# Kernel tuning notes

Hardware: AMD Instinct MI355X
Metric: run time of the kernel (lower is better)

The kernel has to match this reference:

```python
import jax, jax.numpy as jnp
import numpy as np

B, NX, NY = 16, 1024, 1024


def _grad(f, axis):
    # torch.gradient(f, dim=axis, edge_order=2), unit spacing
    fm = jnp.moveaxis(f, axis, -1)
    g = (jnp.roll(fm, -1, -1) - jnp.roll(fm, 1, -1)) * 0.5
    g0 = (-3.0 * fm[..., 0] + 4.0 * fm[..., 1] - fm[..., 2]) * 0.5
    gN = (3.0 * fm[..., -1] - 4.0 * fm[..., -2] + fm[..., -3]) * 0.5
    g = g.at[..., 0].set(g0).at[..., -1].set(gN)
    return jnp.moveaxis(g, -1, axis)


def _grad2(f, axis):
    # roll-based second derivative with one-sided 2nd-order boundary stencils
    fm = jnp.moveaxis(f, axis, -1)
    g = jnp.roll(fm, -1, -1) - 2.0 * fm + jnp.roll(fm, 1, -1)
    g0 = 2.0 * fm[..., 0] - 5.0 * fm[..., 1] + 4.0 * fm[..., 2] - fm[..., 3]
    gN = 2.0 * fm[..., -1] - 5.0 * fm[..., -2] + 4.0 * fm[..., -3] - fm[..., -4]
    g = g.at[..., 0].set(g0).at[..., -1].set(gN)
    return jnp.moveaxis(g, -1, axis)


def setup_inputs() -> dict:
    key = jax.random.key(0)
    k1, k2, k3, k4 = jax.random.split(key, 4)
    f = jax.random.uniform(k1, (B, NX, NY), dtype=jnp.float32)
    A_grid = jax.random.normal(k2, (2, NX, NY), dtype=jnp.float32)
    B_grid = jax.random.uniform(k3, (3, NX, NY), dtype=jnp.float32)
    dt = jax.random.uniform(k4, (B,), dtype=jnp.float32)
    return {"f": f, "A_grid": A_grid, "B_grid": B_grid, "dt": dt}


def reference(f, A_grid, B_grid, dt):
    # Af: [B,2,NX,NY], Bf: [B,3,NX,NY]
    Af = A_grid[None] * f[:, None]
    Bf = B_grid[None] * f[:, None]
    gradv_Af = _grad(Af[:, 0], 1) + _grad(Af[:, 1], 2)
    gradvv_Bf = (
        _grad2(Bf[:, 0], 1)
        + _grad2(Bf[:, 1], 2)
        + _grad(_grad(Bf[:, 2], 2), 1)
        + _grad(_grad(Bf[:, 2], 1), 2)
    )
    df = -gradv_Af + gradvv_Bf * 0.5
    f_new = f + df * dt[:, None, None]
    # ensure_non_negative_f=True
    return jnp.maximum(f_new, 0.0)
```

## Files before the change

### kernel.cpp

```cpp
#include <hip/hip_runtime.h>

#define BATCH 16
#define NX 1024
#define NY 1024
#define CHUNK 8
#define NB 2
#define PLANE (NX * NY)

typedef float v4f __attribute__((ext_vector_type(4)));

struct RawS { v4f a0, a1, b0, b1, b2; float a1l, b1l, b2l, a1r, b1r, b2r; };
struct RawF { v4f f; float fl, fr; };
struct Halo { float a1m, b1m, b2m, a1p, b1p, b2p; };
struct Row  { float pa[4], rr[4], tt[4], fc[4], yc[4]; };

__device__ __forceinline__ RawS load_rawS(int xx, int y0, int tid,
    const float* __restrict__ A0, const float* __restrict__ A1,
    const float* __restrict__ B0, const float* __restrict__ B1,
    const float* __restrict__ B2)
{
    const int base = xx * NY + y0;
    RawS r;
    r.a0 = *(const v4f*)(A0 + base);
    r.a1 = *(const v4f*)(A1 + base);
    r.b0 = *(const v4f*)(B0 + base);
    r.b1 = *(const v4f*)(B1 + base);
    r.b2 = *(const v4f*)(B2 + base);
    const int lane = tid & 63;
    const bool nl = (lane == 0)  && (tid > 0);
    const bool nr = (lane == 63) && (tid < 255);
    r.a1l = nl ? A1[base - 1] : 0.0f;
    r.b1l = nl ? B1[base - 1] : 0.0f;
    r.b2l = nl ? B2[base - 1] : 0.0f;
    r.a1r = nr ? A1[base + 4] : 0.0f;
    r.b1r = nr ? B1[base + 4] : 0.0f;
    r.b2r = nr ? B2[base + 4] : 0.0f;
    return r;
}

__device__ __forceinline__ RawF load_rawF(int xx, int y0, int tid,
    const float* __restrict__ fb)
{
    const int base = xx * NY + y0;
    RawF r;
    r.f = *(const v4f*)(fb + base);
    const int lane = tid & 63;
    const bool nl = (lane == 0)  && (tid > 0);
    const bool nr = (lane == 63) && (tid < 255);
    r.fl = nl ? fb[base - 1] : 0.0f;
    r.fr = nr ? fb[base + 4] : 0.0f;
    return r;
}

__device__ __forceinline__ Halo make_halo(const RawS& rs, int tid)
{
    const int lane = tid & 63;
    Halo h;
    h.a1m = __shfl_up(rs.a1.w, 1);   h.b1m = __shfl_up(rs.b1.w, 1);
    h.b2m = __shfl_up(rs.b2.w, 1);
    h.a1p = __shfl_down(rs.a1.x, 1); h.b1p = __shfl_down(rs.b1.x, 1);
    h.b2p = __shfl_down(rs.b2.x, 1);
    if (lane == 0)  { h.a1m = rs.a1l; h.b1m = rs.b1l; h.b2m = rs.b2l; }
    if (lane == 63) { h.a1p = rs.a1r; h.b1p = rs.b1r; h.b2p = rs.b2r; }
    return h;
}

__device__ __forceinline__ Row convert(const RawS& rs, const Halo& h,
                                       const RawF& rf, int tid)
{
    const int lane = tid & 63;
    float fm = __shfl_up(rf.f.w, 1);
    float fp = __shfl_down(rf.f.x, 1);
    if (lane == 0)  fm = rf.fl;
    if (lane == 63) fp = rf.fr;

    const float qe[6] = { h.a1m * fm, rs.a1.x * rf.f.x, rs.a1.y * rf.f.y,
                          rs.a1.z * rf.f.z, rs.a1.w * rf.f.w, h.a1p * fp };
    const float se[6] = { h.b1m * fm, rs.b1.x * rf.f.x, rs.b1.y * rf.f.y,
                          rs.b1.z * rf.f.z, rs.b1.w * rf.f.w, h.b1p * fp };
    const float te[6] = { h.b2m * fm, rs.b2.x * rf.f.x, rs.b2.y * rf.f.y,
                          rs.b2.z * rf.f.z, rs.b2.w * rf.f.w, h.b2p * fp };

    Row o;
    o.fc[0] = rf.f.x; o.fc[1] = rf.f.y; o.fc[2] = rf.f.z; o.fc[3] = rf.f.w;
    o.pa[0] = rs.a0.x * rf.f.x; o.pa[1] = rs.a0.y * rf.f.y;
    o.pa[2] = rs.a0.z * rf.f.z; o.pa[3] = rs.a0.w * rf.f.w;
    o.rr[0] = rs.b0.x * rf.f.x; o.rr[1] = rs.b0.y * rf.f.y;
    o.rr[2] = rs.b0.z * rf.f.z; o.rr[3] = rs.b0.w * rf.f.w;

    #pragma unroll
    for (int i = 0; i < 4; ++i) {
        const float dq  = 0.5f * (qe[i + 2] - qe[i]);
        const float d2s = se[i + 2] - 2.0f * se[i + 1] + se[i];
        o.tt[i] = 0.5f * (te[i + 2] - te[i]);
        o.yc[i] = -dq + 0.5f * d2s;
    }
    if (tid == 0) {
        const float dq  = 0.5f * (-3.0f * qe[1] + 4.0f * qe[2] - qe[3]);
        const float d2s = 2.0f * se[1] - 5.0f * se[2] + 4.0f * se[3] - se[4];
        o.tt[0] = 0.5f * (-3.0f * te[1] + 4.0f * te[2] - te[3]);
        o.yc[0] = -dq + 0.5f * d2s;
    }
    if (tid == 255) {
        const float dq  = 0.5f * (3.0f * qe[4] - 4.0f * qe[3] + qe[2]);
        const float d2s = 2.0f * se[4] - 5.0f * se[3] + 4.0f * se[2] - se[1];
        o.tt[3] = 0.5f * (3.0f * te[4] - 4.0f * te[3] + te[2]);
        o.yc[3] = -dq + 0.5f * d2s;
    }
    return o;
}

__global__ __launch_bounds__(256) void fp2d_kernel(
    const float* __restrict__ f,
    const float* __restrict__ Ag,
    const float* __restrict__ Bg,
    const float* __restrict__ dt,
    float* __restrict__ out)
{
    const int tid = threadIdx.x;
    const int y0  = tid * 4;
    const int x0  = blockIdx.x * CHUNK;
    const int bb  = blockIdx.y * NB;

    const float* __restrict__ A0 = Ag;
    const float* __restrict__ A1 = Ag + PLANE;
    const float* __restrict__ B0 = Bg;
    const float* __restrict__ B1 = Bg + PLANE;
    const float* __restrict__ B2 = Bg + 2 * PLANE;

    const float* fb[NB];
    float* ob[NB];
    float dtb[NB];
    #pragma unroll
    for (int j = 0; j < NB; ++j) {
        fb[j]  = f   + (size_t)(bb + j) * PLANE;
        ob[j]  = out + (size_t)(bb + j) * PLANE;
        dtb[j] = dt[bb + j];
    }

    const int cs = (x0 == 0) ? 1 : x0;
    const int ce = (x0 + CHUNK == NX) ? NX - 2 : x0 + CHUNK - 1;

    {
    }
    RawS sM = load_rawS(cs - 1, y0, tid, A0, A1, B0, B1, B2);
    RawS sC = load_rawS(cs,     y0, tid, A0, A1, B0, B1, B2);
    RawS sP = load_rawS(cs + 1, y0, tid, A0, A1, B0, B1, B2);
    RawF fM[NB], fC[NB], fP[NB];
    #pragma unroll
    for (int j = 0; j < NB; ++j) {
        fM[j] = load_rawF(cs - 1, y0, tid, fb[j]);
        fC[j] = load_rawF(cs,     y0, tid, fb[j]);
        fP[j] = load_rawF(cs + 1, y0, tid, fb[j]);
    }
    Halo hM = make_halo(sM, tid);
    Halo hC = make_halo(sC, tid);
    Row m[NB], c[NB];
    #pragma unroll
    for (int j = 0; j < NB; ++j) {
        m[j] = convert(sM, hM, fM[j], tid);
        c[j] = convert(sC, hC, fC[j], tid);
    }

    for (int x = cs; x <= ce; ++x) {
        const int xn = (x + 2 < NX) ? x + 2 : NX - 1;
        RawS sN = load_rawS(xn, y0, tid, A0, A1, B0, B1, B2);
        RawF fN[NB];
        #pragma unroll
        for (int j = 0; j < NB; ++j) fN[j] = load_rawF(xn, y0, tid, fb[j]);

        Halo hP = make_halo(sP, tid);
        #pragma unroll
        for (int j = 0; j < NB; ++j) {
            Row p = convert(sP, hP, fP[j], tid);
            v4f o;
            #pragma unroll
            for (int i = 0; i < 4; ++i) {
                const float dxP   = 0.5f * (p.pa[i] - m[j].pa[i]);
                const float dxxR  = p.rr[i] - 2.0f * c[j].rr[i] + m[j].rr[i];
                const float dxdyT = 0.5f * (p.tt[i] - m[j].tt[i]);
                const float df = -dxP + c[j].yc[i] + 0.5f * dxxR + dxdyT;
                o[i] = fmaxf(c[j].fc[i] + df * dtb[j], 0.0f);
            }
            __builtin_nontemporal_store(o, (v4f*)(ob[j] + x * NY + y0));
            m[j] = c[j]; c[j] = p;
        }
        sP = sN;
        #pragma unroll
        for (int j = 0; j < NB; ++j) fP[j] = fN[j];
    }

    if (x0 == 0) {
        RawS s0 = load_rawS(0, y0, tid, A0, A1, B0, B1, B2);
        RawS s1 = load_rawS(1, y0, tid, A0, A1, B0, B1, B2);
        RawS s2 = load_rawS(2, y0, tid, A0, A1, B0, B1, B2);
        RawS s3 = load_rawS(3, y0, tid, A0, A1, B0, B1, B2);
        Halo h0 = make_halo(s0, tid), h1 = make_halo(s1, tid);
        Halo h2 = make_halo(s2, tid), h3 = make_halo(s3, tid);
        #pragma unroll
        for (int j = 0; j < NB; ++j) {
            Row r0 = convert(s0, h0, load_rawF(0, y0, tid, fb[j]), tid);
            Row r1 = convert(s1, h1, load_rawF(1, y0, tid, fb[j]), tid);
            Row r2 = convert(s2, h2, load_rawF(2, y0, tid, fb[j]), tid);
            Row r3 = convert(s3, h3, load_rawF(3, y0, tid, fb[j]), tid);
            v4f o;
            #pragma unroll
            for (int i = 0; i < 4; ++i) {
                const float dxP   = 0.5f * (-3.0f * r0.pa[i] + 4.0f * r1.pa[i] - r2.pa[i]);
                const float dxxR  = 2.0f * r0.rr[i] - 5.0f * r1.rr[i] + 4.0f * r2.rr[i] - r3.rr[i];
                const float dxdyT = 0.5f * (-3.0f * r0.tt[i] + 4.0f * r1.tt[i] - r2.tt[i]);
                const float df = -dxP + r0.yc[i] + 0.5f * dxxR + dxdyT;
                o[i] = fmaxf(r0.fc[i] + df * dtb[j], 0.0f);
            }
            __builtin_nontemporal_store(o, (v4f*)(ob[j] + y0));
        }
    }

    if (x0 + CHUNK == NX) {
        RawS s0 = load_rawS(NX - 1, y0, tid, A0, A1, B0, B1, B2);
        RawS s1 = load_rawS(NX - 2, y0, tid, A0, A1, B0, B1, B2);
        RawS s2 = load_rawS(NX - 3, y0, tid, A0, A1, B0, B1, B2);
        RawS s3 = load_rawS(NX - 4, y0, tid, A0, A1, B0, B1, B2);
        Halo h0 = make_halo(s0, tid), h1 = make_halo(s1, tid);
        Halo h2 = make_halo(s2, tid), h3 = make_halo(s3, tid);
        #pragma unroll
        for (int j = 0; j < NB; ++j) {
            Row r0 = convert(s0, h0, load_rawF(NX - 1, y0, tid, fb[j]), tid);
            Row r1 = convert(s1, h1, load_rawF(NX - 2, y0, tid, fb[j]), tid);
            Row r2 = convert(s2, h2, load_rawF(NX - 3, y0, tid, fb[j]), tid);
            Row r3 = convert(s3, h3, load_rawF(NX - 4, y0, tid, fb[j]), tid);
            v4f o;
            #pragma unroll
            for (int i = 0; i < 4; ++i) {
                const float dxP   = 0.5f * (3.0f * r0.pa[i] - 4.0f * r1.pa[i] + r2.pa[i]);
                const float dxxR  = 2.0f * r0.rr[i] - 5.0f * r1.rr[i] + 4.0f * r2.rr[i] - r3.rr[i];
                const float dxdyT = 0.5f * (3.0f * r0.tt[i] - 4.0f * r1.tt[i] + r2.tt[i]);
                const float df = -dxP + r0.yc[i] + 0.5f * dxxR + dxdyT;
                o[i] = fmaxf(r0.fc[i] + df * dtb[j], 0.0f);
            }
            __builtin_nontemporal_store(o, (v4f*)(ob[j] + (NX - 1) * NY + y0));
        }
    }
}

extern "C" void kernel_launch(void* const* d_in, const int* in_sizes, int n_in,
                              void* d_out, int out_size, void* d_ws, size_t ws_size,
                              hipStream_t stream) {
    const float* f  = (const float*)d_in[0];
    const float* Ag = (const float*)d_in[1];
    const float* Bg = (const float*)d_in[2];
    const float* dt = (const float*)d_in[3];
    float* out = (float*)d_out;

    dim3 block(256, 1, 1);
    dim3 grid(NX / CHUNK, BATCH / NB, 1);
    fp2d_kernel<<<grid, block, 0, stream>>>(f, Ag, Bg, dt, out);
}
```

Baseline: 147.5 us.

## Refactor stencil into per-row coefficient form with direct halo loads

Recasts the interior stencil algebraically: per grid row it precomputes combined coefficients from A/B once, shared across the batch, then produces three partial contributions per f row (ep, es, en) that are summed across x with a single fma. This cuts the per-element multiplies and the carried state. Halo values are now loaded directly from memory with clamped indices instead of using wave shuffles plus lane-edge fallback loads, and f is read with nontemporal loads. The risks are more scalar global loads per row, extra coefficient registers, and slightly different floating-point rounding from the reassociated sums.

New measurement: 169.6 us. 15.0% more time.

```diff
diff --git a/kernel.cpp b/kernel.cpp
--- a/kernel.cpp
+++ b/kernel.cpp
@@ -9,85 +9,117 @@
 
 typedef float v4f __attribute__((ext_vector_type(4)));
 
-struct RawS { v4f a0, a1, b0, b1, b2; float a1l, b1l, b2l, a1r, b1r, b2r; };
-struct RawF { v4f f; float fl, fr; };
-struct Halo { float a1m, b1m, b2m, a1p, b1p, b2p; };
-struct Row  { float pa[4], rr[4], tt[4], fc[4], yc[4]; };
-
-__device__ __forceinline__ RawS load_rawS(int xx, int y0, int tid,
+struct RawG { v4f a0, a1, b0, b1, b2; float a1m, a1p, b1m, b1p, b2m, b2p; };
+struct RawFv { v4f f; float fm, fp; };
+struct Coef { float cp[4], cm[4], c0x[4], xp[4], xm[4], b2w[6], K[4], T[3]; };
+struct RowI { float ep[4], es[4], en[4], fc[4]; };
+struct RowB { float pa[4], rr[4], tt[4], yc[4], fc[4]; };
+
+__device__ __forceinline__ RawG load_rawG(int xx, int y0, int ymo, int ypo,
     const float* __restrict__ A0, const float* __restrict__ A1,
     const float* __restrict__ B0, const float* __restrict__ B1,
     const float* __restrict__ B2)
 {
-    const int base = xx * NY + y0;
-    RawS r;
-    r.a0 = *(const v4f*)(A0 + base);
-    r.a1 = *(const v4f*)(A1 + base);
-    r.b0 = *(const v4f*)(B0 + base);
-    r.b1 = *(const v4f*)(B1 + base);
-    r.b2 = *(const v4f*)(B2 + base);
-    const int lane = tid & 63;
-    const bool nl = (lane == 0)  && (tid > 0);
-    const bool nr = (lane == 63) && (tid < 255);
-    r.a1l = nl ? A1[base - 1] : 0.0f;
-    r.b1l = nl ? B1[base - 1] : 0.0f;
-    r.b2l = nl ? B2[base - 1] : 0.0f;
-    r.a1r = nr ? A1[base + 4] : 0.0f;
-    r.b1r = nr ? B1[base + 4] : 0.0f;
-    r.b2r = nr ? B2[base + 4] : 0.0f;
+    const int b = xx * NY;
+    RawG r;
+    r.a0 = *(const v4f*)(A0 + b + y0);
+    r.a1 = *(const v4f*)(A1 + b + y0);
+    r.b0 = *(const v4f*)(B0 + b + y0);
+    r.b1 = *(const v4f*)(B1 + b + y0);
+    r.b2 = *(const v4f*)(B2 + b + y0);
+    r.a1m = A1[b + ymo]; r.b1m = B1[b + ymo]; r.b2m = B2[b + ymo];
+    r.a1p = A1[b + ypo]; r.b1p = B1[b + ypo]; r.b2p = B2[b + ypo];
     return r;
 }
 
-__device__ __forceinline__ RawF load_rawF(int xx, int y0, int tid,
-    const float* __restrict__ fb)
-{
-    const int base = xx * NY + y0;
-    RawF r;
-    r.f = *(const v4f*)(fb + base);
-    const int lane = tid & 63;
-    const bool nl = (lane == 0)  && (tid > 0);
-    const bool nr = (lane == 63) && (tid < 255);
-    r.fl = nl ? fb[base - 1] : 0.0f;
-    r.fr = nr ? fb[base + 4] : 0.0f;
+__device__ __forceinline__ RawFv load_f(int xx, int y0, int ymo, int ypo,
+                                        const float* __restrict__ fb)
+{
+    const int b = xx * NY;
+    RawFv r;
+    r.f  = __builtin_nontemporal_load((const v4f*)(fb + b + y0));
+    r.fm = __builtin_nontemporal_load(fb + b + ymo);
+    r.fp = __builtin_nontemporal_load(fb + b + ypo);
     return r;
 }
 
-__device__ __forceinline__ Halo make_halo(const RawS& rs, int tid)
-{
-    const int lane = tid & 63;
-    Halo h;
-    h.a1m = __shfl_up(rs.a1.w, 1);   h.b1m = __shfl_up(rs.b1.w, 1);
-    h.b2m = __shfl_up(rs.b2.w, 1);
-    h.a1p = __shfl_down(rs.a1.x, 1); h.b1p = __shfl_down(rs.b1.x, 1);
-    h.b2p = __shfl_down(rs.b2.x, 1);
-    if (lane == 0)  { h.a1m = rs.a1l; h.b1m = rs.b1l; h.b2m = rs.b2l; }
-    if (lane == 63) { h.a1p = rs.a1r; h.b1p = rs.b1r; h.b2p = rs.b2r; }
-    return h;
-}
-
-__device__ __forceinline__ Row convert(const RawS& rs, const Halo& h,
-                                       const RawF& rf, int tid)
-{
-    const int lane = tid & 63;
-    float fm = __shfl_up(rf.f.w, 1);
-    float fp = __shfl_down(rf.f.x, 1);
-    if (lane == 0)  fm = rf.fl;
-    if (lane == 63) fp = rf.fr;
-
-    const float qe[6] = { h.a1m * fm, rs.a1.x * rf.f.x, rs.a1.y * rf.f.y,
-                          rs.a1.z * rf.f.z, rs.a1.w * rf.f.w, h.a1p * fp };
-    const float se[6] = { h.b1m * fm, rs.b1.x * rf.f.x, rs.b1.y * rf.f.y,
-                          rs.b1.z * rf.f.z, rs.b1.w * rf.f.w, h.b1p * fp };
-    const float te[6] = { h.b2m * fm, rs.b2.x * rf.f.x, rs.b2.y * rf.f.y,
-                          rs.b2.z * rf.f.z, rs.b2.w * rf.f.w, h.b2p * fp };
-
-    Row o;
-    o.fc[0] = rf.f.x; o.fc[1] = rf.f.y; o.fc[2] = rf.f.z; o.fc[3] = rf.f.w;
-    o.pa[0] = rs.a0.x * rf.f.x; o.pa[1] = rs.a0.y * rf.f.y;
-    o.pa[2] = rs.a0.z * rf.f.z; o.pa[3] = rs.a0.w * rf.f.w;
-    o.rr[0] = rs.b0.x * rf.f.x; o.rr[1] = rs.b0.y * rf.f.y;
-    o.rr[2] = rs.b0.z * rf.f.z; o.rr[3] = rs.b0.w * rf.f.w;
-
+__device__ __forceinline__ Coef make_coef(const RawG& g, int tid)
+{
+    Coef c;
+    const float a1w[6] = { g.a1m, g.a1.x, g.a1.y, g.a1.z, g.a1.w, g.a1p };
+    const float b1w[6] = { g.b1m, g.b1.x, g.b1.y, g.b1.z, g.b1.w, g.b1p };
+    c.b2w[0] = g.b2m; c.b2w[1] = g.b2.x; c.b2w[2] = g.b2.y;
+    c.b2w[3] = g.b2.z; c.b2w[4] = g.b2.w; c.b2w[5] = g.b2p;
+    #pragma unroll
+    for (int e = 0; e < 4; ++e) {
+        c.xp[e]  = 0.5f * (g.b0[e] - g.a0[e]);
+        c.xm[e]  = 0.5f * (g.b0[e] + g.a0[e]);
+        c.c0x[e] = -(g.b0[e] + b1w[e + 1]);
+        c.cp[e]  = 0.5f * (b1w[e + 2] - a1w[e + 2]);
+        c.cm[e]  = 0.5f * (a1w[e]     + b1w[e]);
+    }
+    if (tid == 0) {
+        c.K[0] = -g.b0.x + 1.5f * g.a1.x + g.b1.x;
+        c.K[1] = -2.0f * g.a1.y - 2.5f * g.b1.y;
+        c.K[2] =  0.5f * g.a1.z + 2.0f * g.b1.z;
+        c.K[3] = -0.5f * g.b1.w;
+        c.T[0] = -0.75f * g.b2.x; c.T[1] = g.b2.y; c.T[2] = -0.25f * g.b2.z;
+    }
+    if (tid == 255) {
+        c.K[0] = -g.b0.w - 1.5f * g.a1.w + g.b1.w;
+        c.K[1] =  2.0f * g.a1.z - 2.5f * g.b1.z;
+        c.K[2] = -0.5f * g.a1.y + 2.0f * g.b1.y;
+        c.K[3] = -0.5f * g.b1.x;
+        c.T[0] = 0.75f * g.b2.w; c.T[1] = -g.b2.z; c.T[2] = 0.25f * g.b2.y;
+    }
+    return c;
+}
+
+__device__ __forceinline__ RowI convertI(const Coef& cf, const RawFv& rf, int tid)
+{
+    const float fw[6] = { rf.fm, rf.f.x, rf.f.y, rf.f.z, rf.f.w, rf.fp };
+    float te[6];
+    #pragma unroll
+    for (int w = 0; w < 6; ++w) te[w] = cf.b2w[w] * fw[w];
+    RowI o;
+    #pragma unroll
+    for (int e = 0; e < 4; ++e) {
+        const float d = 0.25f * (te[e + 2] - te[e]);
+        o.fc[e] = fw[e + 1];
+        o.ep[e] = fw[e + 1] * cf.xp[e]  + d;
+        o.en[e] = fw[e + 1] * cf.xm[e]  - d;
+        o.es[e] = fw[e + 1] * cf.c0x[e] + cf.cp[e] * fw[e + 2] + cf.cm[e] * fw[e];
+    }
+    if (tid == 0) {
+        o.es[0] = cf.K[0] * fw[1] + cf.K[1] * fw[2] + cf.K[2] * fw[3] + cf.K[3] * fw[4];
+        const float h = cf.T[0] * fw[1] + cf.T[1] * fw[2] + cf.T[2] * fw[3];
+        o.ep[0] = fw[1] * cf.xp[0] + h;
+        o.en[0] = fw[1] * cf.xm[0] - h;
+    }
+    if (tid == 255) {
+        o.es[3] = cf.K[0] * fw[4] + cf.K[1] * fw[3] + cf.K[2] * fw[2] + cf.K[3] * fw[1];
+        const float h = cf.T[0] * fw[4] + cf.T[1] * fw[3] + cf.T[2] * fw[2];
+        o.ep[3] = fw[4] * cf.xp[3] + h;
+        o.en[3] = fw[4] * cf.xm[3] - h;
+    }
+    return o;
+}
+
+__device__ __forceinline__ RowB convertB(const RawG& g, const RawFv& rf, int tid)
+{
+    const float fw[6] = { rf.fm, rf.f.x, rf.f.y, rf.f.z, rf.f.w, rf.fp };
+    const float qe[6] = { g.a1m * fw[0], g.a1.x * fw[1], g.a1.y * fw[2],
+                          g.a1.z * fw[3], g.a1.w * fw[4], g.a1p * fw[5] };
+    const float se[6] = { g.b1m * fw[0], g.b1.x * fw[1], g.b1.y * fw[2],
+                          g.b1.z * fw[3], g.b1.w * fw[4], g.b1p * fw[5] };
+    const float te[6] = { g.b2m * fw[0], g.b2.x * fw[1], g.b2.y * fw[2],
+                          g.b2.z * fw[3], g.b2.w * fw[4], g.b2p * fw[5] };
+    RowB o;
+    o.fc[0] = fw[1]; o.fc[1] = fw[2]; o.fc[2] = fw[3]; o.fc[3] = fw[4];
+    o.pa[0] = g.a0.x * fw[1]; o.pa[1] = g.a0.y * fw[2];
+    o.pa[2] = g.a0.z * fw[3]; o.pa[3] = g.a0.w * fw[4];
+    o.rr[0] = g.b0.x * fw[1]; o.rr[1] = g.b0.y * fw[2];
+    o.rr[2] = g.b0.z * fw[3]; o.rr[3] = g.b0.w * fw[4];
     #pragma unroll
     for (int i = 0; i < 4; ++i) {
         const float dq  = 0.5f * (qe[i + 2] - qe[i]);
@@ -119,6 +151,8 @@
 {
     const int tid = threadIdx.x;
     const int y0  = tid * 4;
+    const int ymo = (tid == 0)   ? y0     : y0 - 1;
+    const int ypo = (tid == 255) ? y0 + 3 : y0 + 4;
     const int x0  = blockIdx.x * CHUNK;
     const int bb  = blockIdx.y * NB;
 
@@ -141,104 +175,113 @@
     const int cs = (x0 == 0) ? 1 : x0;
     const int ce = (x0 + CHUNK == NX) ? NX - 2 : x0 + CHUNK - 1;
 
+    float mEn[NB][4], cEs[NB][4], cEn[NB][4], cFc[NB][4];
+
+    RawG gP;
+    RawFv fP[NB];
     {
-    }
-    RawS sM = load_rawS(cs - 1, y0, tid, A0, A1, B0, B1, B2);
-    RawS sC = load_rawS(cs,     y0, tid, A0, A1, B0, B1, B2);
-    RawS sP = load_rawS(cs + 1, y0, tid, A0, A1, B0, B1, B2);
-    RawF fM[NB], fC[NB], fP[NB];
-    #pragma unroll
-    for (int j = 0; j < NB; ++j) {
-        fM[j] = load_rawF(cs - 1, y0, tid, fb[j]);
-        fC[j] = load_rawF(cs,     y0, tid, fb[j]);
-        fP[j] = load_rawF(cs + 1, y0, tid, fb[j]);
-    }
-    Halo hM = make_halo(sM, tid);
-    Halo hC = make_halo(sC, tid);
-    Row m[NB], c[NB];
-    #pragma unroll
-    for (int j = 0; j < NB; ++j) {
-        m[j] = convert(sM, hM, fM[j], tid);
-        c[j] = convert(sC, hC, fC[j], tid);
+        RawG gM = load_rawG(cs - 1, y0, ymo, ypo, A0, A1, B0, B1, B2);
+        RawG gC = load_rawG(cs,     y0, ymo, ypo, A0, A1, B0, B1, B2);
+        gP      = load_rawG(cs + 1, y0, ymo, ypo, A0, A1, B0, B1, B2);
+        const Coef cfM = make_coef(gM, tid);
+        const Coef cfC = make_coef(gC, tid);
+        #pragma unroll
+        for (int j = 0; j < NB; ++j) {
+            RawFv fMj = load_f(cs - 1, y0, ymo, ypo, fb[j]);
+            RawFv fCj = load_f(cs,     y0, ymo, ypo, fb[j]);
+            fP[j]     = load_f(cs + 1, y0, ymo, ypo, fb[j]);
+            RowI rm = convertI(cfM, fMj, tid);
+            RowI rc = convertI(cfC, fCj, tid);
+            #pragma unroll
+            for (int i = 0; i < 4; ++i) {
+                mEn[j][i] = rm.en[i];
+                cEs[j][i] = rc.es[i]; cEn[j][i] = rc.en[i]; cFc[j][i] = rc.fc[i];
+            }
+        }
     }
 
     for (int x = cs; x <= ce; ++x) {
         const int xn = (x + 2 < NX) ? x + 2 : NX - 1;
-        RawS sN = load_rawS(xn, y0, tid, A0, A1, B0, B1, B2);
-        RawF fN[NB];
-        #pragma unroll
-        for (int j = 0; j < NB; ++j) fN[j] = load_rawF(xn, y0, tid, fb[j]);
-
-        Halo hP = make_halo(sP, tid);
+        RawG gN = load_rawG(xn, y0, ymo, ypo, A0, A1, B0, B1, B2);
+        RawFv fN[NB];
+        #pragma unroll
+        for (int j = 0; j < NB; ++j) fN[j] = load_f(xn, y0, ymo, ypo, fb[j]);
+
+        const Coef cf = make_coef(gP, tid);
         #pragma unroll
         for (int j = 0; j < NB; ++j) {
-            Row p = convert(sP, hP, fP[j], tid);
+            RowI rp = convertI(cf, fP[j], tid);
             v4f o;
             #pragma unroll
             for (int i = 0; i < 4; ++i) {
-                const float dxP   = 0.5f * (p.pa[i] - m[j].pa[i]);
-                const float dxxR  = p.rr[i] - 2.0f * c[j].rr[i] + m[j].rr[i];
-                const float dxdyT = 0.5f * (p.tt[i] - m[j].tt[i]);
-                const float df = -dxP + c[j].yc[i] + 0.5f * dxxR + dxdyT;
-                o[i] = fmaxf(c[j].fc[i] + df * dtb[j], 0.0f);
+                const float t = rp.ep[i] + cEs[j][i] + mEn[j][i];
+                o[i] = fmaxf(fmaf(t, dtb[j], cFc[j][i]), 0.0f);
             }
             __builtin_nontemporal_store(o, (v4f*)(ob[j] + x * NY + y0));
-            m[j] = c[j]; c[j] = p;
-        }
-        sP = sN;
+            #pragma unroll
+            for (int i = 0; i < 4; ++i) {
+                mEn[j][i] = cEn[j][i];
+                cEs[j][i] = rp.es[i]; cEn[j][i] = rp.en[i]; cFc[j][i] = rp.fc[i];
+            }
+        }
+        gP = gN;
         #pragma unroll
         for (int j = 0; j < NB; ++j) fP[j] = fN[j];
     }
 
     if (x0 == 0) {
-        RawS s0 = load_rawS(0, y0, tid, A0, A1, B0, B1, B2);
-        RawS s1 = load_rawS(1, y0, tid, A0, A1, B0, B1, B2);
-        RawS s2 = load_rawS(2, y0, tid, A0, A1, B0, B1, B2);
-        RawS s3 = load_rawS(3, y0, tid, A0, A1, B0, B1, B2);
-        Halo h0 = make_halo(s0, tid), h1 = make_halo(s1, tid);
-        Halo h2 = make_halo(s2, tid), h3 = make_halo(s3, tid);
+        const float wPx[4] = {  1.5f, -2.0f,  0.5f,  0.0f };
+        const float wRx[4] = {  1.0f, -2.5f,  2.0f, -0.5f };
+        const float wTx[4] = { -1.5f,  2.0f, -0.5f,  0.0f };
+        float acc[NB][4], fc0[NB][4];
+        #pragma unroll
+        for (int r = 0; r < 4; ++r) {
+            RawG g = load_rawG(r, y0, ymo, ypo, A0, A1, B0, B1, B2);
+            #pragma unroll
+            for (int j = 0; j < NB; ++j) {
+                RowB rb = convertB(g, load_f(r, y0, ymo, ypo, fb[j]), tid);
+                #pragma unroll
+                for (int i = 0; i < 4; ++i) {
+                    if (r == 0) { acc[j][i] = rb.yc[i]; fc0[j][i] = rb.fc[i]; }
+                    acc[j][i] += wPx[r] * rb.pa[i] + wRx[r] * rb.rr[i] + wTx[r] * rb.tt[i];
+                }
+            }
+        }
         #pragma unroll
         for (int j = 0; j < NB; ++j) {
-            Row r0 = convert(s0, h0, load_rawF(0, y0, tid, fb[j]), tid);
-            Row r1 = convert(s1, h1, load_rawF(1, y0, tid, fb[j]), tid);
-            Row r2 = convert(s2, h2, load_rawF(2, y0, tid, fb[j]), tid);
-            Row r3 = convert(s3, h3, load_rawF(3, y0, tid, fb[j]), tid);
             v4f o;
             #pragma unroll
-            for (int i = 0; i < 4; ++i) {
-                const float dxP   = 0.5f * (-3.0f * r0.pa[i] + 4.0f * r1.pa[i] - r2.pa[i]);
-                const float dxxR  = 2.0f * r0.rr[i] - 5.0f * r1.rr[i] + 4.0f * r2.rr[i] - r3.rr[i];
-                const float dxdyT = 0.5f * (-3.0f * r0.tt[i] + 4.0f * r1.tt[i] - r2.tt[i]);
-                const float df = -dxP + r0.yc[i] + 0.5f * dxxR + dxdyT;
-                o[i] = fmaxf(r0.fc[i] + df * dtb[j], 0.0f);
-            }
+            for (int i = 0; i < 4; ++i)
+                o[i] = fmaxf(fmaf(acc[j][i], dtb[j], fc0[j][i]), 0.0f);
             __builtin_nontemporal_store(o, (v4f*)(ob[j] + y0));
         }
     }
 
     if (x0 + CHUNK == NX) {
-        RawS s0 = load_rawS(NX - 1, y0, tid, A0, A1, B0, B1, B2);
-        RawS s1 = load_rawS(NX - 2, y0, tid, A0, A1, B0, B1, B2);
-        RawS s2 = load_rawS(NX - 3, y0, tid, A0, A1, B0, B1, B2);
-        RawS s3 = load_rawS(NX - 4, y0, tid, A0, A1, B0, B1, B2);
-        Halo h0 = make_halo(s0, tid), h1 = make_halo(s1, tid);
-        Halo h2 = make_halo(s2, tid), h3 = make_halo(s3, tid);
+        const float wPx[4] = { -1.5f,  2.0f, -0.5f,  0.0f };
+        const float wRx[4] = {  1.0f, -2.5f,  2.0f, -0.5f };
+        const float wTx[4] = {  1.5f, -2.0f,  0.5f,  0.0f };
+        float acc[NB][4], fc0[NB][4];
+        #pragma unroll
+        for (int r = 0; r < 4; ++r) {
+            RawG g = load_rawG(NX - 1 - r, y0, ymo, ypo, A0, A1, B0, B1, B2);
+            #pragma unroll
+            for (int j = 0; j < NB; ++j) {
+                RowB rb = convertB(g, load_f(NX - 1 - r, y0, ymo, ypo, fb[j]), tid);
+                #pragma unroll
+                for (int i = 0; i < 4; ++i) {
+                    if (r == 0) { acc[j][i] = rb.yc[i]; fc0[j][i] = rb.fc[i]; }
+                    acc[j][i] += wPx[r] * rb.pa[i] + wRx[r] * rb.rr[i] + wTx[r] * rb.tt[i];
+                }
+            }
+        }
         #pragma unroll
         for (int j = 0; j < NB; ++j) {
-            Row r0 = convert(s0, h0, load_rawF(NX - 1, y0, tid, fb[j]), tid);
-            Row r1 = convert(s1, h1, load_rawF(NX - 2, y0, tid, fb[j]), tid);
-            Row r2 = convert(s2, h2, load_rawF(NX - 3, y0, tid, fb[j]), tid);
-            Row r3 = convert(s3, h3, load_rawF(NX - 4, y0, tid, fb[j]), tid);
             v4f o;
             #pragma unroll
-            for (int i = 0; i < 4; ++i) {
-                const float dxP   = 0.5f * (3.0f * r0.pa[i] - 4.0f * r1.pa[i] + r2.pa[i]);
-                const float dxxR  = 2.0f * r0.rr[i] - 5.0f * r1.rr[i] + 4.0f * r2.rr[i] - r3.rr[i];
-                const float dxdyT = 0.5f * (3.0f * r0.tt[i] - 4.0f * r1.tt[i] + r2.tt[i]);
-                const float df = -dxP + r0.yc[i] + 0.5f * dxxR + dxdyT;
-                o[i] = fmaxf(r0.fc[i] + df * dtb[j], 0.0f);
-            }
-            __builtin_nontemporal_store(o, (v4f*)(ob[j] + (NX - 1) * NY + y0));
+            for (int i = 0; i < 4; ++i)
+                o[i] = fmaxf(fmaf(acc[j][i], dtb[j], fc0[j][i]), 0.0f);
+            __builtin_nontemporal_store(o, (v4f*)(ob[j] + (size_t)(NX - 1) * NY + y0));
         }
     }
 }
```
